# Optimization experiments

Hardware: AMD Instinct MI355X
Metric: run time of the kernel (lower is better)

## Reference

```python
import jax, jax.numpy as jnp
import numpy as np


def _severity_weights():
    # class order: Black=0, Blue=1, Green=2, TTR=3; rows = true class, cols = pred class
    return jnp.array([[0., 4., 5., 2.],
                      [5., 0., 3., 1.],
                      [5., 3., 0., 2.],
                      [3., 2., 2., 0.]], dtype=jnp.float32)


def setup_inputs() -> dict:
    key = jax.random.key(0)
    k1, k2 = jax.random.split(key)
    B, C = 8388608, 4
    outputs = jax.random.normal(k1, (B, C), dtype=jnp.float32)
    targets = jax.random.randint(k2, (B,), 0, C, dtype=jnp.int64)
    return {"outputs": outputs, "targets": targets, "weights": _severity_weights()}


def reference(outputs, targets, weights):
    # argmax of softmax == argmax of logits
    preds = jnp.argmax(outputs, axis=1)
    severity = weights[targets, preds]                       # [B] gather
    logp = jax.nn.log_softmax(outputs, axis=1)               # [B, 4]
    ce = -jnp.take_along_axis(logp, targets[:, None], axis=1)[:, 0]
    return (severity + ce).mean()
```

## Files before the change

kernel.cpp:

```cpp
#include <hip/hip_runtime.h>
#include <hip/hip_bf16.h>

#define BLOCK 256
#define GRID 2048

__global__ __launch_bounds__(BLOCK) void wcl_main_kernel(
    const float4* __restrict__ out4,
    const int*    __restrict__ tgt,
    const float*  __restrict__ w,
    double*       __restrict__ acc,
    int B)
{
    __shared__ float sw[16];
    __shared__ float wave_sums[BLOCK / 64];

    if (threadIdx.x < 16) sw[threadIdx.x] = w[threadIdx.x];
    __syncthreads();

    float local = 0.0f;
    const int stride = gridDim.x * blockDim.x;
    for (int i = blockIdx.x * blockDim.x + threadIdx.x; i < B; i += stride) {
        const float4 x = out4[i];
        const int t = tgt[i];

        float best = x.x; int pred = 0;
        if (x.y > best) { best = x.y; pred = 1; }
        if (x.z > best) { best = x.z; pred = 2; }
        if (x.w > best) { best = x.w; pred = 3; }

        const float sev = sw[t * 4 + pred];

        const float s = expf(x.x - best) + expf(x.y - best) +
                        expf(x.z - best) + expf(x.w - best);
        const float lse = best + logf(s);
        const float xt = (t == 0) ? x.x : (t == 1) ? x.y : (t == 2) ? x.z : x.w;

        local += sev + (lse - xt);
    }

    #pragma unroll
    for (int off = 32; off > 0; off >>= 1)
        local += __shfl_down(local, off);

    const int lane = threadIdx.x & 63;
    const int wave = threadIdx.x >> 6;
    if (lane == 0) wave_sums[wave] = local;
    __syncthreads();

    if (threadIdx.x == 0) {
        float bsum = 0.0f;
        #pragma unroll
        for (int i = 0; i < BLOCK / 64; ++i) bsum += wave_sums[i];
        atomicAdd(acc, (double)bsum);
    }
}

__global__ void wcl_final_kernel(const double* __restrict__ acc,
                                 float* __restrict__ out, int B)
{
    out[0] = (float)(acc[0] / (double)B);
}

extern "C" void kernel_launch(void* const* d_in, const int* in_sizes, int n_in,
                              void* d_out, int out_size, void* d_ws, size_t ws_size,
                              hipStream_t stream) {
    const float* outputs = (const float*)d_in[0];
    const int*   targets = (const int*)d_in[1];
    const float* weights = (const float*)d_in[2];
    const int B = in_sizes[0] / 4;

    double* acc = (double*)d_ws;
    hipMemsetAsync(d_ws, 0, sizeof(double), stream);

    wcl_main_kernel<<<GRID, BLOCK, 0, stream>>>(
        (const float4*)outputs, targets, weights, acc, B);
    wcl_final_kernel<<<1, 1, 0, stream>>>(acc, (float*)d_out, B);
}
```

Baseline: 224.4 us.

## Unroll grid-stride loop with nontemporal loads and replace atomics with partials reduction

Unrolls the main grid-stride loop by four using nontemporal vector loads for logits and targets, so each thread keeps more memory requests in flight. Replaces the per-block double atomicAdd and the memset launch with a per-block partials array reduced by a one-block final kernel. This adds workspace use and ties the final reduction to the fixed GRID constant.

```diff
diff --git a/kernel.cpp b/kernel.cpp
--- a/kernel.cpp
+++ b/kernel.cpp
@@ -4,11 +4,26 @@
 #define BLOCK 256
 #define GRID 2048
 
+typedef float floatx4 __attribute__((ext_vector_type(4)));
+
+__device__ __forceinline__ float row_loss(floatx4 x, int t, const float* sw) {
+    float best = x.x; int pred = 0;
+    if (x.y > best) { best = x.y; pred = 1; }
+    if (x.z > best) { best = x.z; pred = 2; }
+    if (x.w > best) { best = x.w; pred = 3; }
+    const float sev = sw[t * 4 + pred];
+    const float s = expf(x.x - best) + expf(x.y - best) +
+                    expf(x.z - best) + expf(x.w - best);
+    const float lse = best + logf(s);
+    const float xt = (t == 0) ? x.x : (t == 1) ? x.y : (t == 2) ? x.z : x.w;
+    return sev + (lse - xt);
+}
+
 __global__ __launch_bounds__(BLOCK) void wcl_main_kernel(
-    const float4* __restrict__ out4,
-    const int*    __restrict__ tgt,
-    const float*  __restrict__ w,
-    double*       __restrict__ acc,
+    const floatx4* __restrict__ out4,
+    const int*     __restrict__ tgt,
+    const float*   __restrict__ w,
+    float*         __restrict__ partials,
     int B)
 {
     __shared__ float sw[16];
@@ -17,25 +32,30 @@
     if (threadIdx.x < 16) sw[threadIdx.x] = w[threadIdx.x];
     __syncthreads();
 
+    const int stride = GRID * BLOCK;
+    int i = blockIdx.x * BLOCK + threadIdx.x;
+
     float local = 0.0f;
-    const int stride = gridDim.x * blockDim.x;
-    for (int i = blockIdx.x * blockDim.x + threadIdx.x; i < B; i += stride) {
-        const float4 x = out4[i];
-        const int t = tgt[i];
-
-        float best = x.x; int pred = 0;
-        if (x.y > best) { best = x.y; pred = 1; }
-        if (x.z > best) { best = x.z; pred = 2; }
-        if (x.w > best) { best = x.w; pred = 3; }
-
-        const float sev = sw[t * 4 + pred];
-
-        const float s = expf(x.x - best) + expf(x.y - best) +
-                        expf(x.z - best) + expf(x.w - best);
-        const float lse = best + logf(s);
-        const float xt = (t == 0) ? x.x : (t == 1) ? x.y : (t == 2) ? x.z : x.w;
-
-        local += sev + (lse - xt);
+    while (i + 3 * stride < B) {
+        floatx4 x0 = __builtin_nontemporal_load(&out4[i]);
+        floatx4 x1 = __builtin_nontemporal_load(&out4[i + stride]);
+        floatx4 x2 = __builtin_nontemporal_load(&out4[i + 2 * stride]);
+        floatx4 x3 = __builtin_nontemporal_load(&out4[i + 3 * stride]);
+        int t0 = __builtin_nontemporal_load(&tgt[i]);
+        int t1 = __builtin_nontemporal_load(&tgt[i + stride]);
+        int t2 = __builtin_nontemporal_load(&tgt[i + 2 * stride]);
+        int t3 = __builtin_nontemporal_load(&tgt[i + 3 * stride]);
+        local += row_loss(x0, t0, sw);
+        local += row_loss(x1, t1, sw);
+        local += row_loss(x2, t2, sw);
+        local += row_loss(x3, t3, sw);
+        i += 4 * stride;
+    }
+    while (i < B) {
+        floatx4 x = __builtin_nontemporal_load(&out4[i]);
+        int t = __builtin_nontemporal_load(&tgt[i]);
+        local += row_loss(x, t, sw);
+        i += stride;
     }
 
     #pragma unroll
@@ -50,15 +70,34 @@
     if (threadIdx.x == 0) {
         float bsum = 0.0f;
         #pragma unroll
-        for (int i = 0; i < BLOCK / 64; ++i) bsum += wave_sums[i];
-        atomicAdd(acc, (double)bsum);
+        for (int j = 0; j < BLOCK / 64; ++j) bsum += wave_sums[j];
+        partials[blockIdx.x] = bsum;
     }
 }
 
-__global__ void wcl_final_kernel(const double* __restrict__ acc,
-                                 float* __restrict__ out, int B)
+__global__ __launch_bounds__(BLOCK) void wcl_final_kernel(
+    const float* __restrict__ partials, float* __restrict__ out, int B)
 {
-    out[0] = (float)(acc[0] / (double)B);
+    __shared__ double wave_sums[BLOCK / 64];
+    double local = 0.0;
+    for (int i = threadIdx.x; i < GRID; i += BLOCK)
+        local += (double)partials[i];
+
+    #pragma unroll
+    for (int off = 32; off > 0; off >>= 1)
+        local += __shfl_down(local, off);
+
+    const int lane = threadIdx.x & 63;
+    const int wave = threadIdx.x >> 6;
+    if (lane == 0) wave_sums[wave] = local;
+    __syncthreads();
+
+    if (threadIdx.x == 0) {
+        double s = 0.0;
+        #pragma unroll
+        for (int j = 0; j < BLOCK / 64; ++j) s += wave_sums[j];
+        out[0] = (float)(s / (double)B);
+    }
 }
 
 extern "C" void kernel_launch(void* const* d_in, const int* in_sizes, int n_in,
@@ -69,10 +108,9 @@
     const float* weights = (const float*)d_in[2];
     const int B = in_sizes[0] / 4;
 
-    double* acc = (double*)d_ws;
-    hipMemsetAsync(d_ws, 0, sizeof(double), stream);
+    float* partials = (float*)d_ws;
 
     wcl_main_kernel<<<GRID, BLOCK, 0, stream>>>(
-        (const float4*)outputs, targets, weights, acc, B);
-    wcl_final_kernel<<<1, 1, 0, stream>>>(acc, (float*)d_out, B);
+        (const floatx4*)outputs, targets, weights, partials, B);
+    wcl_final_kernel<<<1, BLOCK, 0, stream>>>(partials, (float*)d_out, B);
 }
```

After: 207.6 us. 7.5% less time.
